# Performance work log

Hardware: AMD Instinct MI355X
Metric: run time of the kernel (lower is better)

The kernel has to match this reference:

```python
import jax, jax.numpy as jnp
import numpy as np

N_NODES = 100000
D_IN, D_OUT = 1024, 512
B, K = 8192, 64


def setup_inputs() -> dict:
    key = jax.random.key(0)
    k1, k2, k3, k4, k5 = jax.random.split(key, 5)
    X = jax.random.normal(k1, (N_NODES, D_IN), dtype=jnp.float32)
    indices = jax.random.randint(k2, (B, K), 0, N_NODES)  # top-K PPR neighbor ids per batch node
    values = jax.random.uniform(k3, (B, K), dtype=jnp.float32)  # PPR weights
    W = jax.random.normal(k4, (D_IN, D_OUT), dtype=jnp.float32) / np.sqrt(D_IN)
    b = jax.random.normal(k5, (D_OUT,), dtype=jnp.float32)
    return {"X": X, "indices": indices, "values": values, "W": W, "b": b}


def reference(X, indices, values, W, b):
    # Sparse PPR branch. Original: encode only unique gathered rows, then
    # re-expand via inverse indices. Since the encoder is row-pointwise,
    # encoder(X[u_fwd])[u_bwd] == encoder(X)[indices]; we encode all nodes once
    # (n_nodes < B*K here) then gather -- identical math, jit-friendly.
    enc = X @ W + b                      # [N, d_out]
    gathered = enc[indices]              # [B, K, d_out]
    return jnp.einsum('bk,bkd->bd', values, gathered)  # weighted sum over K neighbors
```

## Files before the change

kernel.cpp:

```cpp
#include <hip/hip_runtime.h>

typedef unsigned short ushort_t;
typedef __bf16 bf16x8 __attribute__((ext_vector_type(8)));
typedef float f32x4 __attribute__((ext_vector_type(4)));

#define N_NODES 100000
#define M_PAD   100096
#define D_IN    1024
#define D_OUT   512
#define B_SZ    8192
#define K_NB    64

__device__ __forceinline__ ushort_t f2bf(float f) {
    unsigned int u = __builtin_bit_cast(unsigned int, f);
    u += 0x7FFFu + ((u >> 16) & 1u);
    return (ushort_t)(u >> 16);
}
__device__ __forceinline__ float bflo(unsigned d) {
    return __builtin_bit_cast(float, d << 16);
}
__device__ __forceinline__ float bfhi(unsigned d) {
    return __builtin_bit_cast(float, d & 0xFFFF0000u);
}

__device__ __forceinline__ void gload16(const ushort_t* g, ushort_t* l) {
    __builtin_amdgcn_global_load_lds(
        (const __attribute__((address_space(1))) void*)g,
        (__attribute__((address_space(3))) void*)l,
        16, 0, 0);
}

__global__ __launch_bounds__(256) void cast_w_kernel(
        const float* __restrict__ W, ushort_t* __restrict__ Wt) {
    int o = blockIdx.x * 256 + threadIdx.x;
    int n = o >> 10;
    int k = o & 1023;
    Wt[o] = f2bf(W[k * D_OUT + n]);
}

__global__ __launch_bounds__(256) void cast_x_kernel(
        const float* __restrict__ X, ushort_t* __restrict__ Xb) {
    size_t o = ((size_t)blockIdx.x * 256 + threadIdx.x) * 8;
    float4 a = *(const float4*)(X + o);
    float4 b = *(const float4*)(X + o + 4);
    uint4 r;
    r.x = (unsigned)f2bf(a.x) | ((unsigned)f2bf(a.y) << 16);
    r.y = (unsigned)f2bf(a.z) | ((unsigned)f2bf(a.w) << 16);
    r.z = (unsigned)f2bf(b.x) | ((unsigned)f2bf(b.y) << 16);
    r.w = (unsigned)f2bf(b.z) | ((unsigned)f2bf(b.w) << 16);
    *(uint4*)(Xb + o) = r;
}

__global__ __launch_bounds__(256) void encode_gemm_kernel(
        const ushort_t* __restrict__ Xb, const ushort_t* __restrict__ Wt,
        const float* __restrict__ bias, ushort_t* __restrict__ Enc) {
    int m0 = blockIdx.x * 128;
    int n0 = blockIdx.y * 128;
    int t = threadIdx.x;
    int lane = t & 63;
    int wave = t >> 6;
    int wm = (wave >> 1) * 64;
    int wn = (wave & 1) * 64;
    int quad = lane >> 4;
    int l16  = lane & 15;

    __shared__ __align__(16) ushort_t As[128 * 32];
    __shared__ __align__(16) ushort_t Bs[128 * 32];

    f32x4 acc[4][4];
    f32x4 zero = {0.f, 0.f, 0.f, 0.f};
    #pragma unroll
    for (int i = 0; i < 4; i++)
        #pragma unroll
        for (int j = 0; j < 4; j++)
            acc[i][j] = zero;

    const ushort_t* ga = Xb + (size_t)(m0 + (t >> 2)) * D_IN + (t & 3) * 8;
    const ushort_t* gb = Wt + (size_t)(n0 + (t >> 2)) * D_IN + (t & 3) * 8;
    ushort_t* la = As + t * 8;
    ushort_t* lb = Bs + t * 8;
    const size_t rowskip = (size_t)64 * D_IN;

    for (int k0 = 0; k0 < D_IN; k0 += 32) {
        gload16(ga + k0,           la);
        gload16(ga + rowskip + k0, la + 2048);
        gload16(gb + k0,           lb);
        gload16(gb + rowskip + k0, lb + 2048);
        __syncthreads();

        bf16x8 a[4], b[4];
        #pragma unroll
        for (int i = 0; i < 4; i++) {
            a[i] = *(const bf16x8*)(As + (wm + i * 16 + l16) * 32 + quad * 8);
            b[i] = *(const bf16x8*)(Bs + (wn + i * 16 + l16) * 32 + quad * 8);
        }
        #pragma unroll
        for (int i = 0; i < 4; i++)
            #pragma unroll
            for (int j = 0; j < 4; j++)
                acc[i][j] = __builtin_amdgcn_mfma_f32_16x16x32_bf16(
                                a[i], b[j], acc[i][j], 0, 0, 0);
        __syncthreads();
    }

    float bv[4];
    #pragma unroll
    for (int j = 0; j < 4; j++) bv[j] = bias[n0 + wn + j * 16 + l16];

    #pragma unroll
    for (int i = 0; i < 4; i++) {
        #pragma unroll
        for (int r = 0; r < 4; r++) {
            int grow = m0 + wm + i * 16 + quad * 4 + r;
            if (grow < N_NODES) {
                #pragma unroll
                for (int j = 0; j < 4; j++) {
                    int gcol = n0 + wn + j * 16 + l16;
                    Enc[(size_t)grow * D_OUT + gcol] = f2bf(acc[i][j][r] + bv[j]);
                }
            }
        }
    }
}

__global__ __launch_bounds__(256) void gather_out_kernel(
        const ushort_t* __restrict__ Enc, const int* __restrict__ idx,
        const float* __restrict__ val, float* __restrict__ out) {
    int b = blockIdx.x;
    int t = threadIdx.x;

    __shared__ int   sidx[K_NB];
    __shared__ float sval[K_NB];
    __shared__ float part[8 * 3 * 64];
    if (t < K_NB) {
        sidx[t] = idx[b * K_NB + t];
        sval[t] = val[b * K_NB + t];
    }
    __syncthreads();

    int h = t >> 6;
    int c = t & 63;

    float acc[8] = {0.f, 0.f, 0.f, 0.f, 0.f, 0.f, 0.f, 0.f};

    uint4 x[8];
    #pragma unroll
    for (int u = 0; u < 8; u++)
        x[u] = ((const uint4*)(Enc + (size_t)sidx[h + 4 * u] * D_OUT))[c];

    #pragma unroll
    for (int j0 = 0; j0 < 16; j0 += 8) {
        uint4 cur[8];
        #pragma unroll
        for (int u = 0; u < 8; u++) cur[u] = x[u];
        if (j0 + 8 < 16) {
            #pragma unroll
            for (int u = 0; u < 8; u++)
                x[u] = ((const uint4*)(
                    Enc + (size_t)sidx[h + 4 * (j0 + 8 + u)] * D_OUT))[c];
        }
        #pragma unroll
        for (int u = 0; u < 8; u++) {
            float v = sval[h + 4 * (j0 + u)];
            acc[0] = fmaf(v, bflo(cur[u].x), acc[0]);
            acc[1] = fmaf(v, bfhi(cur[u].x), acc[1]);
            acc[2] = fmaf(v, bflo(cur[u].y), acc[2]);
            acc[3] = fmaf(v, bfhi(cur[u].y), acc[3]);
            acc[4] = fmaf(v, bflo(cur[u].z), acc[4]);
            acc[5] = fmaf(v, bfhi(cur[u].z), acc[5]);
            acc[6] = fmaf(v, bflo(cur[u].w), acc[6]);
            acc[7] = fmaf(v, bfhi(cur[u].w), acc[7]);
        }
    }

    if (h != 0) {
        #pragma unroll
        for (int e = 0; e < 8; e++)
            part[e * 192 + (h - 1) * 64 + c] = acc[e];
    }
    __syncthreads();
    if (h == 0) {
        float r[8];
        #pragma unroll
        for (int e = 0; e < 8; e++)
            r[e] = acc[e] + part[e * 192 + c] + part[e * 192 + 64 + c]
                          + part[e * 192 + 128 + c];
        float4 o0 = {r[0], r[1], r[2], r[3]};
        float4 o1 = {r[4], r[5], r[6], r[7]};
        float* dst = out + (size_t)b * D_OUT + c * 8;
        *(float4*)(dst)     = o0;
        *(float4*)(dst + 4) = o1;
    }
}

__global__ __launch_bounds__(256) void gather_f32_kernel(
        const float* __restrict__ X, const int* __restrict__ idx,
        const float* __restrict__ val, ushort_t* __restrict__ Y,
        float* __restrict__ s) {
    int b = blockIdx.x;
    int t = threadIdx.x;

    __shared__ int   sidx[K_NB];
    __shared__ float sval[K_NB];
    if (t < K_NB) {
        sidx[t] = idx[b * K_NB + t];
        sval[t] = val[b * K_NB + t];
    }
    __syncthreads();

    float ax = 0.f, ay = 0.f, az = 0.f, aw = 0.f;
    #pragma unroll 8
    for (int k = 0; k < K_NB; k++) {
        const float4* row = (const float4*)(X + (size_t)sidx[k] * D_IN);
        float4 x = row[t];
        float  v = sval[k];
        ax = fmaf(v, x.x, ax);
        ay = fmaf(v, x.y, ay);
        az = fmaf(v, x.z, az);
        aw = fmaf(v, x.w, aw);
    }
    uint2 o;
    o.x = (unsigned)f2bf(ax) | ((unsigned)f2bf(ay) << 16);
    o.y = (unsigned)f2bf(az) | ((unsigned)f2bf(aw) << 16);
    *(uint2*)(Y + (size_t)b * D_IN + t * 4) = o;

    if (t == 0) {
        float sum = 0.f;
        #pragma unroll
        for (int k = 0; k < K_NB; k++) sum += sval[k];
        s[b] = sum;
    }
}

__global__ __launch_bounds__(256) void gemm_kernel(
        const ushort_t* __restrict__ Y, const ushort_t* __restrict__ Wt,
        const float* __restrict__ s, const float* __restrict__ bias,
        float* __restrict__ out) {
    const int Kdim = D_IN;
    int m0 = blockIdx.x * 128;
    int n0 = blockIdx.y * 128;
    int t = threadIdx.x;
    int lane = t & 63;
    int wave = t >> 6;
    int wm = (wave >> 1) * 64;
    int wn = (wave & 1) * 64;
    int quad = lane >> 4;
    int l16  = lane & 15;

    __shared__ __align__(16) ushort_t As[128 * 32];
    __shared__ __align__(16) ushort_t Bs[128 * 32];

    f32x4 acc[4][4];
    f32x4 zero = {0.f, 0.f, 0.f, 0.f};
    #pragma unroll
    for (int i = 0; i < 4; i++)
        #pragma unroll
        for (int j = 0; j < 4; j++)
            acc[i][j] = zero;

    int rsw = (l16 >> 2) & 3;

    for (int k0 = 0; k0 < Kdim; k0 += 32) {
        #pragma unroll
        for (int i = 0; i < 2; i++) {
            int c   = t + i * 256;
            int row = c >> 2;
            int chk = c & 3;
            int pos = chk ^ ((row >> 2) & 3);
            *(int4*)(As + row * 32 + pos * 8) =
                *(const int4*)(Y + (size_t)(m0 + row) * Kdim + k0 + chk * 8);
            *(int4*)(Bs + row * 32 + pos * 8) =
                *(const int4*)(Wt + (size_t)(n0 + row) * Kdim + k0 + chk * 8);
        }
        __syncthreads();

        bf16x8 a[4], b[4];
        int rchk = quad ^ rsw;
        #pragma unroll
        for (int i = 0; i < 4; i++) {
            a[i] = *(const bf16x8*)(As + (wm + i * 16 + l16) * 32 + rchk * 8);
            b[i] = *(const bf16x8*)(Bs + (wn + i * 16 + l16) * 32 + rchk * 8);
        }
        #pragma unroll
        for (int i = 0; i < 4; i++)
            #pragma unroll
            for (int j = 0; j < 4; j++)
                acc[i][j] = __builtin_amdgcn_mfma_f32_16x16x32_bf16(
                                a[i], b[j], acc[i][j], 0, 0, 0);
        __syncthreads();
    }

    #pragma unroll
    for (int i = 0; i < 4; i++) {
        #pragma unroll
        for (int r = 0; r < 4; r++) {
            int grow = m0 + wm + i * 16 + quad * 4 + r;
            float sv = s[grow];
            #pragma unroll
            for (int j = 0; j < 4; j++) {
                int gcol = n0 + wn + j * 16 + l16;
                out[(size_t)grow * D_OUT + gcol] = acc[i][j][r] + sv * bias[gcol];
            }
        }
    }
}

extern "C" void kernel_launch(void* const* d_in, const int* in_sizes, int n_in,
                              void* d_out, int out_size, void* d_ws, size_t ws_size,
                              hipStream_t stream) {
    const float* X    = (const float*)d_in[0];
    const int*   idx  = (const int*)d_in[1];
    const float* val  = (const float*)d_in[2];
    const float* W    = (const float*)d_in[3];
    const float* bias = (const float*)d_in[4];
    float* out = (float*)d_out;

    const size_t XB_BYTES  = (size_t)M_PAD * D_IN * 2;
    const size_t ENC_BYTES = (size_t)M_PAD * D_OUT * 2;
    const size_t WT_BYTES  = (size_t)D_OUT * D_IN * 2;
    const size_t Y_BYTES   = (size_t)B_SZ * D_IN * 2;
    const size_t S_BYTES   = (size_t)B_SZ * 4;

    char* ws = (char*)d_ws;
    bool fast = ws_size >= XB_BYTES + ENC_BYTES + WT_BYTES;

    if (fast) {
        ushort_t* Xb  = (ushort_t*)ws;
        ushort_t* Enc = (ushort_t*)(ws + XB_BYTES);
        ushort_t* Wt  = (ushort_t*)(ws + XB_BYTES + ENC_BYTES);

        hipLaunchKernelGGL(cast_w_kernel, dim3((D_OUT * D_IN) / 256), dim3(256),
                           0, stream, W, Wt);
        hipLaunchKernelGGL(cast_x_kernel, dim3((N_NODES * D_IN) / (256 * 8)),
                           dim3(256), 0, stream, X, Xb);
        hipLaunchKernelGGL(encode_gemm_kernel, dim3(M_PAD / 128, D_OUT / 128),
                           dim3(256), 0, stream, Xb, Wt, bias, Enc);
        hipLaunchKernelGGL(gather_out_kernel, dim3(B_SZ), dim3(256),
                           0, stream, Enc, idx, val, out);
    } else {
        ushort_t* Yb = (ushort_t*)ws;
        ushort_t* Wt = (ushort_t*)(ws + Y_BYTES);
        float*    sb = (float*)(ws + Y_BYTES + WT_BYTES);

        hipLaunchKernelGGL(cast_w_kernel, dim3((D_OUT * D_IN) / 256), dim3(256),
                           0, stream, W, Wt);
        hipLaunchKernelGGL(gather_f32_kernel, dim3(B_SZ), dim3(256),
                           0, stream, X, idx, val, Yb, sb);
        hipLaunchKernelGGL(gemm_kernel, dim3(B_SZ / 128, D_OUT / 128), dim3(256),
                           0, stream, Yb, Wt, sb, bias, out);
    }
}
```

Measured before the change: 801.8 us.

## Fuse X fp32-to-bf16 cast into encode GEMM with swizzled LDS and block remap

Removes the separate cast_x kernel and the bf16 copy of X, so the GEMM loads fp32 X directly, converts in registers and stores to LDS, with a register prefetch of the next k-slice. It also XOR-swizzles the LDS layout to reduce bank conflicts, and remaps a 1D grid so blocks sharing the same M rows across N tiles land near each other for L2 reuse. The aim is to avoid writing and re-reading the 200MB bf16 X. The trade-off is that the GEMM now reads 4x-replicated fp32 X (once per N tile), which relies on L2/MALL reuse, and the register staging path replaces the async global-to-LDS load for A.

After: 730.1 us. 8.9% less time.

```diff
diff --git a/kernel.cpp b/kernel.cpp
--- a/kernel.cpp
+++ b/kernel.cpp
@@ -30,6 +30,15 @@
         16, 0, 0);
 }
 
+__device__ __forceinline__ bf16x8 pack8(float4 a, float4 b) {
+    bf16x8 r;
+    r[0] = (__bf16)a.x; r[1] = (__bf16)a.y;
+    r[2] = (__bf16)a.z; r[3] = (__bf16)a.w;
+    r[4] = (__bf16)b.x; r[5] = (__bf16)b.y;
+    r[6] = (__bf16)b.z; r[7] = (__bf16)b.w;
+    return r;
+}
+
 __global__ __launch_bounds__(256) void cast_w_kernel(
         const float* __restrict__ W, ushort_t* __restrict__ Wt) {
     int o = blockIdx.x * 256 + threadIdx.x;
@@ -38,24 +47,14 @@
     Wt[o] = f2bf(W[k * D_OUT + n]);
 }
 
-__global__ __launch_bounds__(256) void cast_x_kernel(
-        const float* __restrict__ X, ushort_t* __restrict__ Xb) {
-    size_t o = ((size_t)blockIdx.x * 256 + threadIdx.x) * 8;
-    float4 a = *(const float4*)(X + o);
-    float4 b = *(const float4*)(X + o + 4);
-    uint4 r;
-    r.x = (unsigned)f2bf(a.x) | ((unsigned)f2bf(a.y) << 16);
-    r.y = (unsigned)f2bf(a.z) | ((unsigned)f2bf(a.w) << 16);
-    r.z = (unsigned)f2bf(b.x) | ((unsigned)f2bf(b.y) << 16);
-    r.w = (unsigned)f2bf(b.z) | ((unsigned)f2bf(b.w) << 16);
-    *(uint4*)(Xb + o) = r;
-}
-
 __global__ __launch_bounds__(256) void encode_gemm_kernel(
-        const ushort_t* __restrict__ Xb, const ushort_t* __restrict__ Wt,
+        const float* __restrict__ X, const ushort_t* __restrict__ Wt,
         const float* __restrict__ bias, ushort_t* __restrict__ Enc) {
-    int m0 = blockIdx.x * 128;
-    int n0 = blockIdx.y * 128;
+    int bid = blockIdx.x;
+    int logical = (bid & 7) * 391 + (bid >> 3);
+    int m0 = (logical >> 2) * 128;
+    int n0 = (logical & 3) * 128;
+
     int t = threadIdx.x;
     int lane = t & 63;
     int wave = t >> 6;
@@ -75,24 +74,50 @@
         for (int j = 0; j < 4; j++)
             acc[i][j] = zero;
 
-    const ushort_t* ga = Xb + (size_t)(m0 + (t >> 2)) * D_IN + (t & 3) * 8;
-    const ushort_t* gb = Wt + (size_t)(n0 + (t >> 2)) * D_IN + (t & 3) * 8;
-    ushort_t* la = As + t * 8;
+    int srow = t >> 2;
+    int kch  = t & 3;
+    int schk = kch ^ ((srow >> 2) & 3);
+
+    const ushort_t* gb = Wt + (size_t)(n0 + srow) * D_IN + schk * 8;
     ushort_t* lb = Bs + t * 8;
     const size_t rowskip = (size_t)64 * D_IN;
 
+    int ar0 = m0 + srow;
+    int ar1 = m0 + srow + 64;
+    if (ar0 > N_NODES - 1) ar0 = N_NODES - 1;
+    if (ar1 > N_NODES - 1) ar1 = N_NODES - 1;
+    const float* pa0 = X + (size_t)ar0 * D_IN + kch * 8;
+    const float* pa1 = X + (size_t)ar1 * D_IN + kch * 8;
+    ushort_t* aw0 = As + srow * 32 + schk * 8;
+    ushort_t* aw1 = aw0 + 64 * 32;
+
+    float4 f00 = *(const float4*)(pa0);
+    float4 f01 = *(const float4*)(pa0 + 4);
+    float4 f10 = *(const float4*)(pa1);
+    float4 f11 = *(const float4*)(pa1 + 4);
+
+    int rsw  = (l16 >> 2) & 3;
+    int rchk = quad ^ rsw;
+
     for (int k0 = 0; k0 < D_IN; k0 += 32) {
-        gload16(ga + k0,           la);
-        gload16(ga + rowskip + k0, la + 2048);
+        *(bf16x8*)aw0 = pack8(f00, f01);
+        *(bf16x8*)aw1 = pack8(f10, f11);
         gload16(gb + k0,           lb);
         gload16(gb + rowskip + k0, lb + 2048);
         __syncthreads();
 
+        if (k0 + 32 < D_IN) {
+            f00 = *(const float4*)(pa0 + k0 + 32);
+            f01 = *(const float4*)(pa0 + k0 + 36);
+            f10 = *(const float4*)(pa1 + k0 + 32);
+            f11 = *(const float4*)(pa1 + k0 + 36);
+        }
+
         bf16x8 a[4], b[4];
         #pragma unroll
         for (int i = 0; i < 4; i++) {
-            a[i] = *(const bf16x8*)(As + (wm + i * 16 + l16) * 32 + quad * 8);
-            b[i] = *(const bf16x8*)(Bs + (wn + i * 16 + l16) * 32 + quad * 8);
+            a[i] = *(const bf16x8*)(As + (wm + i * 16 + l16) * 32 + rchk * 8);
+            b[i] = *(const bf16x8*)(Bs + (wn + i * 16 + l16) * 32 + rchk * 8);
         }
         #pragma unroll
         for (int i = 0; i < 4; i++)
@@ -315,26 +340,21 @@
     const float* bias = (const float*)d_in[4];
     float* out = (float*)d_out;
 
-    const size_t XB_BYTES  = (size_t)M_PAD * D_IN * 2;
     const size_t ENC_BYTES = (size_t)M_PAD * D_OUT * 2;
     const size_t WT_BYTES  = (size_t)D_OUT * D_IN * 2;
     const size_t Y_BYTES   = (size_t)B_SZ * D_IN * 2;
-    const size_t S_BYTES   = (size_t)B_SZ * 4;
 
     char* ws = (char*)d_ws;
-    bool fast = ws_size >= XB_BYTES + ENC_BYTES + WT_BYTES;
+    bool fast = ws_size >= ENC_BYTES + WT_BYTES;
 
     if (fast) {
-        ushort_t* Xb  = (ushort_t*)ws;
-        ushort_t* Enc = (ushort_t*)(ws + XB_BYTES);
-        ushort_t* Wt  = (ushort_t*)(ws + XB_BYTES + ENC_BYTES);
+        ushort_t* Enc = (ushort_t*)ws;
+        ushort_t* Wt  = (ushort_t*)(ws + ENC_BYTES);
 
         hipLaunchKernelGGL(cast_w_kernel, dim3((D_OUT * D_IN) / 256), dim3(256),
                            0, stream, W, Wt);
-        hipLaunchKernelGGL(cast_x_kernel, dim3((N_NODES * D_IN) / (256 * 8)),
-                           dim3(256), 0, stream, X, Xb);
-        hipLaunchKernelGGL(encode_gemm_kernel, dim3(M_PAD / 128, D_OUT / 128),
-                           dim3(256), 0, stream, Xb, Wt, bias, Enc);
+        hipLaunchKernelGGL(encode_gemm_kernel, dim3((M_PAD / 128) * (D_OUT / 128)),
+                           dim3(256), 0, stream, X, Wt, bias, Enc);
         hipLaunchKernelGGL(gather_out_kernel, dim3(B_SZ), dim3(256),
                            0, stream, Enc, idx, val, out);
     } else {
```
